# Performance work log

Measured on AMD Instinct MI355X. Metric: run time of the kernel, lower is better.

The kernel has to match this reference:

```python
import jax, jax.numpy as jnp
import numpy as np

N_CONST = 188
P = 16
HIDDEN = 128
DE = 5
DO = 6
N_TARGETS = 5
BATCH = 32


def _edge_indices(n):
    # receiver/sender pairs in the same order as itertools.product, skipping diagonal
    r, s = np.meshgrid(np.arange(n), np.arange(n), indexing='ij')
    mask = r != s
    return jnp.asarray(r[mask]), jnp.asarray(s[mask])  # each [n*(n-1)]


def _linear_params(key, fan_in, fan_out):
    kw, kb = jax.random.split(key)
    w = jax.random.normal(kw, (fan_in, fan_out), jnp.float32) / np.sqrt(fan_in)
    b = jax.random.normal(kb, (fan_out,), jnp.float32) * 0.01
    return w, b


def setup_inputs() -> dict:
    key = jax.random.key(0)
    ks = jax.random.split(key, 10)
    inp = {"x": jax.random.normal(ks[0], (BATCH, N_CONST, P), jnp.float32)}
    h2 = HIDDEN // 2
    dims = [
        ("fr1", 2 * P, HIDDEN), ("fr2", HIDDEN, h2), ("fr3", h2, DE),
        ("fo1", P + DE, HIDDEN), ("fo2", HIDDEN, h2), ("fo3", h2, DO),
        ("fc1", DO * N_CONST, HIDDEN), ("fc2", HIDDEN, h2), ("fc3", h2, N_TARGETS),
    ]
    for i, (name, fi, fo) in enumerate(dims):
        w, b = _linear_params(ks[i + 1], fi, fo)
        inp[name + "_w"] = w
        inp[name + "_b"] = b
    return inp


def reference(x, fr1_w, fr1_b, fr2_w, fr2_b, fr3_w, fr3_b,
              fo1_w, fo1_b, fo2_w, fo2_b, fo3_w, fo3_b,
              fc1_w, fc1_b, fc2_w, fc2_b, fc3_w, fc3_b):
    B, n, p = x.shape
    recv, send = _edge_indices(n)  # [Nr]
    # gather receiver/sender node features (replaces one-hot matmuls with Rr, Rs)
    e_in = jnp.concatenate([x[:, recv], x[:, send]], axis=-1)  # [B, Nr, 2P]
    h = jax.nn.relu(e_in @ fr1_w + fr1_b)
    h = jax.nn.relu(h @ fr2_w + fr2_b)
    E = jax.nn.relu(h @ fr3_w + fr3_b)  # [B, Nr, De]
    # scatter-add edge effects back to receiver nodes (replaces E @ Rr^T)
    Ebar = jnp.zeros((B, n, E.shape[-1]), x.dtype).at[:, recv].add(E)  # [B, N, De]
    c = jnp.concatenate([x, Ebar], axis=-1)  # [B, N, P+De]
    h = jax.nn.relu(c @ fo1_w + fo1_b)
    h = jax.nn.relu(h @ fo2_w + fo2_b)
    O = jax.nn.relu(h @ fo3_w + fo3_b)  # [B, N, Do]
    h = jax.nn.relu(O.reshape(B, -1) @ fc1_w + fc1_b)
    h = jax.nn.relu(h @ fc2_w + fc2_b)
    return h @ fc3_w + fc3_b  # [B, n_targets]
```

## Files before the change

kernel.cpp:

```cpp
#include <hip/hip_runtime.h>

#define BB   32
#define NN   188
#define PP   16
#define HID  128
#define HH2  64
#define DE   5
#define DO   6
#define NT   5
#define ROWS_O (BB*NN)
#define RT   32
#define KO   (PP+DE)

typedef __attribute__((ext_vector_type(8))) short short8;
typedef __attribute__((ext_vector_type(4))) float float4_;
typedef __attribute__((ext_vector_type(4))) unsigned uint4_;

__device__ __forceinline__ short f2bf(float v) {
    union { float f; unsigned u; } a; a.f = v;
    unsigned r = a.u + 0x7fff + ((a.u >> 16) & 1);
    return (short)(r >> 16);
}
__device__ __forceinline__ unsigned relu_pk(float lo, float hi) {
    float l = lo > 0.f ? lo : 0.f;
    float h = hi > 0.f ? hi : 0.f;
    unsigned r;
    asm("v_cvt_pk_bf16_f32 %0, %1, %2" : "=v"(r) : "v"(l), "v"(h));
    return r;
}

#define XB_OFF    0
#define XB_ELTS   (BB*NN*24)
#define W1S_OFF   (XB_OFF + XB_ELTS)
#define W1S_ELTS  (8*64*8)
#define W2S_OFF   (W1S_OFF + W1S_ELTS)
#define W2S_ELTS  (16*64*8)
#define W3S_OFF   (W2S_OFF + W2S_ELTS)
#define W3S_ELTS  (2*64*8)
#define SHORT_TOTAL (W3S_OFF + W3S_ELTS)

__device__ __forceinline__ int kmap(int q, int e) {
    return (e < 4) ? (q*4 + e) : (16 + q*4 + (e - 4));
}

__global__ void prep_kernel(const float* __restrict__ x,
                            const float* __restrict__ w1,
                            const float* __restrict__ w2,
                            const float* __restrict__ w3,
                            short* __restrict__ ws)
{
    const int i = blockIdx.x * blockDim.x + threadIdx.x;
    const int stride = gridDim.x * blockDim.x;
    for (int idx = i; idx < BB*NN*PP; idx += stride) {
        int row = idx >> 4, k = idx & 15;
        ws[XB_OFF + row*24 + k] = f2bf(x[idx]);
    }
    for (int idx = i; idx < W1S_ELTS; idx += stride) {
        int t = idx >> 9;
        int l = (idx >> 3) & 63;
        int e = idx & 7;
        int q = l >> 4, n16 = l & 15;
        ws[W1S_OFF + idx] = f2bf(w1[(q*8 + e)*HID + t*16 + n16]);
    }
    for (int idx = i; idx < W2S_ELTS; idx += stride) {
        int f = idx >> 9;
        int l = (idx >> 3) & 63;
        int e = idx & 7;
        int tt = f >> 2, s = f & 3;
        int q = l >> 4, n16 = l & 15;
        int k = 32*s + kmap(q, e);
        int n = tt*16 + n16;
        ws[W2S_OFF + idx] = f2bf(w2[k*HH2 + n]);
    }
    for (int idx = i; idx < W3S_ELTS; idx += stride) {
        int s2 = idx >> 9;
        int l = (idx >> 3) & 63;
        int e = idx & 7;
        int q = l >> 4, n16 = l & 15;
        int k = 32*s2 + kmap(q, e);
        ws[W3S_OFF + idx] = (n16 < DE) ? f2bf(w3[k*DE + n16]) : (short)0;
    }
}

#define EDGE_TILE(E1C, MASKED, TI)                                              \
    {                                                                           \
        float4_ C2[4];                                                          \
        {    \
            float4_ Ca = __builtin_amdgcn_mfma_f32_16x16x32_bf16(W1f[0], (E1C), cbv[0], 0, 0, 0); \
            float4_ Cb = __builtin_amdgcn_mfma_f32_16x16x32_bf16(W1f[1], (E1C), cbv[1], 0, 0, 0); \
            uint4_ dv = (uint4_){ relu_pk(Ca[0], Ca[1]), relu_pk(Ca[2], Ca[3]),  \
                                  relu_pk(Cb[0], Cb[1]), relu_pk(Cb[2], Cb[3]) };\
            short8 Bf = __builtin_bit_cast(short8, dv);                         \
            C2[0] = __builtin_amdgcn_mfma_f32_16x16x32_bf16(W2f[0],  Bf, bias2v[0], 0, 0, 0); \
            C2[1] = __builtin_amdgcn_mfma_f32_16x16x32_bf16(W2f[4],  Bf, bias2v[1], 0, 0, 0); \
            C2[2] = __builtin_amdgcn_mfma_f32_16x16x32_bf16(W2f[8],  Bf, bias2v[2], 0, 0, 0); \
            C2[3] = __builtin_amdgcn_mfma_f32_16x16x32_bf16(W2f[12], Bf, bias2v[3], 0, 0, 0); \
        }                                                                       \
        _Pragma("unroll")                                                       \
        for (int s = 1; s < 4; ++s) {                                           \
            float4_ Ca = __builtin_amdgcn_mfma_f32_16x16x32_bf16(W1f[2*s],   (E1C), cbv[2*s],   0, 0, 0); \
            float4_ Cb = __builtin_amdgcn_mfma_f32_16x16x32_bf16(W1f[2*s+1], (E1C), cbv[2*s+1], 0, 0, 0); \
            uint4_ dv = (uint4_){ relu_pk(Ca[0], Ca[1]), relu_pk(Ca[2], Ca[3]),  \
                                  relu_pk(Cb[0], Cb[1]), relu_pk(Cb[2], Cb[3]) };\
            short8 Bf = __builtin_bit_cast(short8, dv);                         \
            C2[0] = __builtin_amdgcn_mfma_f32_16x16x32_bf16(W2f[s],    Bf, C2[0], 0, 0, 0); \
            C2[1] = __builtin_amdgcn_mfma_f32_16x16x32_bf16(W2f[4+s],  Bf, C2[1], 0, 0, 0); \
            C2[2] = __builtin_amdgcn_mfma_f32_16x16x32_bf16(W2f[8+s],  Bf, C2[2], 0, 0, 0); \
            C2[3] = __builtin_amdgcn_mfma_f32_16x16x32_bf16(W2f[12+s], Bf, C2[3], 0, 0, 0); \
        }                                                                       \
        float4_ C3;                                                             \
        {               \
            uint4_ dv = (uint4_){ relu_pk(C2[0][0], C2[0][1]), relu_pk(C2[0][2], C2[0][3]), \
                                  relu_pk(C2[1][0], C2[1][1]), relu_pk(C2[1][2], C2[1][3]) }; \
            short8 B3f = __builtin_bit_cast(short8, dv);                        \
            C3 = __builtin_amdgcn_mfma_f32_16x16x32_bf16(W3f[0], B3f, bias3r, 0, 0, 0); \
        }                                                                       \
        {                                                                       \
            uint4_ dv = (uint4_){ relu_pk(C2[2][0], C2[2][1]), relu_pk(C2[2][2], C2[2][3]), \
                                  relu_pk(C2[3][0], C2[3][1]), relu_pk(C2[3][2], C2[3][3]) }; \
            short8 B3f = __builtin_bit_cast(short8, dv);                        \
            C3 = __builtin_amdgcn_mfma_f32_16x16x32_bf16(W3f[1], B3f, C3, 0, 0, 0); \
        }                                                                       \
        if (MASKED) {                       \
            const bool ok = ((TI)*16 + n16 < NN-1);                             \
            _Pragma("unroll")                                                   \
            for (int rg = 0; rg < 4; ++rg) {                                    \
                float v = C3[rg] > 0.f ? C3[rg] : 0.f;                          \
                acc[rg] += ok ? v : 0.f;                                        \
            }                                                                   \
        } else {                                                                \
            _Pragma("unroll")                                                   \
            for (int rg = 0; rg < 4; ++rg)                                      \
                acc[rg] += C3[rg] > 0.f ? C3[rg] : 0.f;                         \
        }                                                                       \
    }

__global__ __launch_bounds__(256) __attribute__((amdgpu_waves_per_eu(2, 2)))
void edge_mfma_kernel(const short* __restrict__ ws_s,
                      const float* __restrict__ b1,
                      const float* __restrict__ b2,
                      const float* __restrict__ b3,
                      float* __restrict__ ebar)
{
    const short* xb  = ws_s + XB_OFF;
    const short* w1g = ws_s + W1S_OFF;
    const short* w2g = ws_s + W2S_OFF;
    const short* w3g = ws_s + W3S_OFF;

    const int tid  = threadIdx.x;
    const int wave = tid >> 6;
    const int lane = tid & 63;
    const int n16  = lane & 15;
    const int q    = lane >> 4;
    const int bi   = blockIdx.x * 4 + wave;
    const int b    = bi / NN;
    const int recv = bi - b*NN;

    short8 W1f[8];
    #pragma unroll
    for (int t = 0; t < 8; ++t)
        W1f[t] = *(const short8*)(w1g + t*512 + lane*8);
    short8 W2f[16];
    #pragma unroll
    for (int f = 0; f < 16; ++f)
        W2f[f] = *(const short8*)(w2g + f*512 + lane*8);
    short8 W3f[2];
    #pragma unroll
    for (int s = 0; s < 2; ++s)
        W3f[s] = *(const short8*)(w3g + s*512 + lane*8);
    float4_ cbv[8];
    #pragma unroll
    for (int t = 0; t < 8; ++t)
        cbv[t] = *(const float4_*)(b1 + t*16 + q*4);
    float4_ bias2v[4];
    #pragma unroll
    for (int tt = 0; tt < 4; ++tt)
        bias2v[tt] = *(const float4_*)(b2 + tt*16 + q*4);
    float4_ bias3r;
    #pragma unroll
    for (int rg = 0; rg < 4; ++rg) {
        int o = q*4 + rg;
        bias3r[rg] = (o < DE) ? b3[o] : 0.f;
    }

    const short* xrow = xb + b*(NN*24);
    const bool rside = (q < 2);

    float acc[4] = {0.f, 0.f, 0.f, 0.f};

    short8 E1;
    {
        int send0 = n16 + (n16 >= recv ? 1 : 0);
        const int node = rside ? recv : send0;
        E1 = *(const short8*)(xrow + node*24 + (q & 1)*8);
    }

    #pragma unroll 1
    for (int ti = 0; ti < 11; ++ti) {
        short8 E1c = E1;
        {
            int en = (ti+1)*16 + n16;
            int send = en + (en >= recv ? 1 : 0);
            if (send > NN-1) send = NN-1;
            const int node = rside ? recv : send;
            E1 = *(const short8*)(xrow + node*24 + (q & 1)*8);
        }
        EDGE_TILE(E1c, false, ti)
    }
    EDGE_TILE(E1, true, 11)

    #pragma unroll
    for (int rg = 0; rg < 4; ++rg) {
        acc[rg] += __shfl_xor(acc[rg], 1);
        acc[rg] += __shfl_xor(acc[rg], 2);
        acc[rg] += __shfl_xor(acc[rg], 4);
        acc[rg] += __shfl_xor(acc[rg], 8);
    }
    if (n16 == 0) {
        #pragma unroll
        for (int rg = 0; rg < 4; ++rg) {
            int o = q*4 + rg;
            if (o < DE) ebar[bi*DE + o] = acc[rg];
        }
    }
}

__global__ __launch_bounds__(512)
void obj_mlp_kernel(const float* __restrict__ x, const float* __restrict__ ebar,
                    const float* __restrict__ w1, const float* __restrict__ b1,
                    const float* __restrict__ w2, const float* __restrict__ b2,
                    const float* __restrict__ w3, const float* __restrict__ b3,
                    float* __restrict__ o_out)
{
    __shared__ float sW[HID*HH2];
    __shared__ float sB1[HID];
    __shared__ float sB2[HH2];
    __shared__ float sCin[RT*KO];
    __shared__ float sH1[RT*HID];
    __shared__ float sH2t[HH2*(RT+1)];
    const int tid = threadIdx.x;
    const int rbase = blockIdx.x * RT;

    for (int i = tid; i < KO*HID; i += 512) sW[i] = w1[i];
    if (tid < HID) sB1[tid] = b1[tid];
    else if (tid < HID+HH2) sB2[tid-HID] = b2[tid-HID];
    for (int i = tid; i < RT*KO; i += 512) {
        int r = i / KO, k = i - r*KO;
        int gr = rbase + r;
        int b = gr / NN;
        int node = gr - b*NN;
        sCin[i] = (k < PP) ? x[(b*NN+node)*PP + k]
                           : ebar[(b*NN+node)*DE + (k-PP)];
    }
    __syncthreads();

    {
        const int j = tid & (HID-1);
        const int g = tid >> 7;
        float w[KO];
        #pragma unroll
        for (int k = 0; k < KO; ++k) w[k] = sW[k*HID + j];
        const float bj = sB1[j];
        #pragma unroll
        for (int rr = 0; rr < 8; ++rr) {
            const int r = g*8 + rr;
            const float* e = &sCin[r*KO];
            float a0=0.f,a1=0.f,a2=0.f;
            #pragma unroll
            for (int k = 0; k < KO; k += 3) {
                a0 += w[k+0]*e[k+0];
                a1 += w[k+1]*e[k+1];
                a2 += w[k+2]*e[k+2];
            }
            float v = a0+a1+a2+bj;
            sH1[r*HID + j] = v > 0.f ? v : 0.f;
        }
    }
    __syncthreads();
    for (int i = tid; i < HID*HH2; i += 512) sW[i] = w2[i];
    __syncthreads();

    {
        const int j = tid & (HH2-1);
        const int g = tid >> 6;
        float acc[4];
        #pragma unroll
        for (int rr = 0; rr < 4; ++rr) acc[rr] = sB2[j];
        #pragma unroll
        for (int kc = 0; kc < HID; kc += 32) {
            float w[32];
            #pragma unroll
            for (int kk = 0; kk < 32; ++kk) w[kk] = sW[(kc+kk)*HH2 + j];
            #pragma unroll
            for (int rr = 0; rr < 4; ++rr) {
                const float* h = &sH1[(g*4+rr)*HID + kc];
                float a0=0.f,a1=0.f,a2=0.f,a3=0.f;
                #pragma unroll
                for (int kk = 0; kk < 32; kk += 4) {
                    a0 += w[kk+0]*h[kk+0];
                    a1 += w[kk+1]*h[kk+1];
                    a2 += w[kk+2]*h[kk+2];
                    a3 += w[kk+3]*h[kk+3];
                }
                acc[rr] += (a0+a1)+(a2+a3);
            }
        }
        #pragma unroll
        for (int rr = 0; rr < 4; ++rr) {
            float v = acc[rr];
            sH2t[j*(RT+1) + (g*4+rr)] = v > 0.f ? v : 0.f;
        }
    }
    __syncthreads();

    if (tid < RT*DO) {
        const int r = tid & (RT-1);
        const int c = tid >> 5;
        float a0=0.f,a1=0.f,a2=0.f,a3=0.f;
        #pragma unroll
        for (int k = 0; k < HH2; k += 4) {
            a0 += sH2t[(k+0)*(RT+1)+r]*w3[(k+0)*DO+c];
            a1 += sH2t[(k+1)*(RT+1)+r]*w3[(k+1)*DO+c];
            a2 += sH2t[(k+2)*(RT+1)+r]*w3[(k+2)*DO+c];
            a3 += sH2t[(k+3)*(RT+1)+r]*w3[(k+3)*DO+c];
        }
        float v = (a0+a1)+(a2+a3) + b3[c];
        v = v > 0.f ? v : 0.f;
        int gr = rbase + r;
        int b = gr / NN;
        int node = gr - b*NN;
        o_out[b*(NN*DO) + node*DO + c] = v;
    }
}

__global__ __launch_bounds__(256)
void fc_kernel(const float* __restrict__ o_in,
               const float* __restrict__ w1, const float* __restrict__ b1,
               const float* __restrict__ w2, const float* __restrict__ b2,
               const float* __restrict__ w3, const float* __restrict__ b3,
               float* __restrict__ out)
{
    __shared__ __align__(16) float s_in[NN*DO];
    __shared__ float s_p[256];
    __shared__ float s_h1[HID];
    __shared__ float s_h2[HH2];
    const int b = blockIdx.x, tid = threadIdx.x;

    for (int i = tid; i < NN*DO; i += 256) s_in[i] = o_in[b*(NN*DO) + i];
    __syncthreads();

    {
        const int j = tid & (HID-1);
        const int h = tid >> 7;
        const float4* s4 = (const float4*)&s_in[h*564];
        const float* wbase = w1 + (size_t)(h*564)*HID + j;
        float a0=0.f,a1=0.f,a2=0.f,a3=0.f;
        #pragma unroll 4
        for (int i = 0; i < 141; ++i) {
            float4 v = s4[i];
            const float* wp = wbase + (size_t)i*4*HID;
            a0 += v.x * wp[0];
            a1 += v.y * wp[HID];
            a2 += v.z * wp[2*HID];
            a3 += v.w * wp[3*HID];
        }
        s_p[tid] = (a0+a1)+(a2+a3);
    }
    __syncthreads();
    if (tid < HID) {
        float v = s_p[tid] + s_p[tid+HID] + b1[tid];
        s_h1[tid] = v > 0.f ? v : 0.f;
    }
    __syncthreads();

    {
        const int j = tid & (HH2-1);
        const int q = tid >> 6;
        float acc = 0.f;
        #pragma unroll
        for (int kk = 0; kk < 32; ++kk) {
            int k = q*32 + kk;
            acc += s_h1[k] * w2[k*HH2 + j];
        }
        s_p[tid] = acc;
    }
    __syncthreads();
    if (tid < HH2) {
        float v = s_p[tid] + s_p[tid+64] + s_p[tid+128] + s_p[tid+192] + b2[tid];
        s_h2[tid] = v > 0.f ? v : 0.f;
    }
    __syncthreads();

    if (tid < NT) {
        float acc = b3[tid];
        #pragma unroll
        for (int k = 0; k < HH2; ++k)
            acc += s_h2[k] * w3[k*NT + tid];
        out[b*NT + tid] = acc;
    }
}

extern "C" void kernel_launch(void* const* d_in, const int* in_sizes, int n_in,
                              void* d_out, int out_size, void* d_ws, size_t ws_size,
                              hipStream_t stream) {
    (void)in_sizes; (void)n_in; (void)out_size; (void)ws_size;
    const float* x     = (const float*)d_in[0];
    const float* fr1_w = (const float*)d_in[1];
    const float* fr1_b = (const float*)d_in[2];
    const float* fr2_w = (const float*)d_in[3];
    const float* fr2_b = (const float*)d_in[4];
    const float* fr3_w = (const float*)d_in[5];
    const float* fr3_b = (const float*)d_in[6];
    const float* fo1_w = (const float*)d_in[7];
    const float* fo1_b = (const float*)d_in[8];
    const float* fo2_w = (const float*)d_in[9];
    const float* fo2_b = (const float*)d_in[10];
    const float* fo3_w = (const float*)d_in[11];
    const float* fo3_b = (const float*)d_in[12];
    const float* fc1_w = (const float*)d_in[13];
    const float* fc1_b = (const float*)d_in[14];
    const float* fc2_w = (const float*)d_in[15];
    const float* fc2_b = (const float*)d_in[16];
    const float* fc3_w = (const float*)d_in[17];
    const float* fc3_b = (const float*)d_in[18];

    short* ws_s = (short*)d_ws;
    size_t fbase = ((size_t)SHORT_TOTAL*2 + 15) & ~(size_t)15;
    float* ebar = (float*)((char*)d_ws + fbase);
    float* o_ws = ebar + BB*NN*DE;

    prep_kernel<<<128, 256, 0, stream>>>(x, fr1_w, fr2_w, fr3_w, ws_s);
    edge_mfma_kernel<<<(BB*NN)/4, 256, 0, stream>>>(ws_s, fr1_b, fr2_b, fr3_b, ebar);
    obj_mlp_kernel<<<ROWS_O/RT, 512, 0, stream>>>(
        x, ebar, fo1_w, fo1_b, fo2_w, fo2_b, fo3_w, fo3_b, o_ws);
    fc_kernel<<<BB, 256, 0, stream>>>(
        o_ws, fc1_w, fc1_b, fc2_w, fc2_b, fc3_w, fc3_b, (float*)d_out);
}
```

Before: 161.2 us.

## Fuse edge, object and fc stages into one persistent kernel with grid barriers

Merges the edge MLP, object MLP and final fc kernels into one persistent kernel of 256 blocks that loops over work and uses software grid-wide barriers built on atomics between stages. The goal is to remove two kernel launches and the gaps between them. In exchange, the edge stage has fewer waves in flight, since each wave now handles up to 6 receivers and the waves_per_eu hint is dropped. The object-MLP stage also shrinks from 32-row tiles on 512 threads to 16-row tiles on 256 threads and reloads its weights into shared memory for every chunk. The grid barrier assumes all 256 blocks are co-resident, which could deadlock if occupancy is insufficient.

Result: slower. 296.8 us (+84.2%).

```diff
diff --git a/kernel.cpp b/kernel.cpp
--- a/kernel.cpp
+++ b/kernel.cpp
@@ -9,8 +9,9 @@
 #define DO   6
 #define NT   5
 #define ROWS_O (BB*NN)
-#define RT   32
+#define RTO  16
 #define KO   (PP+DE)
+#define NBLK 256
 
 typedef __attribute__((ext_vector_type(8))) short short8;
 typedef __attribute__((ext_vector_type(4))) float float4_;
@@ -27,6 +28,9 @@
     unsigned r;
     asm("v_cvt_pk_bf16_f32 %0, %1, %2" : "=v"(r) : "v"(l), "v"(h));
     return r;
+}
+__device__ __forceinline__ float4_ mfma16(short8 a, short8 b, float4_ c) {
+    return __builtin_amdgcn_mfma_f32_16x16x32_bf16(a, b, c, 0, 0, 0);
 }
 
 #define XB_OFF    0
@@ -43,14 +47,34 @@
     return (e < 4) ? (q*4 + e) : (16 + q*4 + (e - 4));
 }
 
+__device__ __forceinline__ void grid_sync(int* bar) {
+    __threadfence();
+    __syncthreads();
+    if (threadIdx.x == 0) {
+        int gen = __hip_atomic_load(bar + 1, __ATOMIC_RELAXED, __HIP_MEMORY_SCOPE_AGENT);
+        int prev = __hip_atomic_fetch_add(bar, 1, __ATOMIC_ACQ_REL, __HIP_MEMORY_SCOPE_AGENT);
+        if (prev == (int)gridDim.x - 1) {
+            __hip_atomic_store(bar, 0, __ATOMIC_RELAXED, __HIP_MEMORY_SCOPE_AGENT);
+            __hip_atomic_fetch_add(bar + 1, 1, __ATOMIC_RELEASE, __HIP_MEMORY_SCOPE_AGENT);
+        } else {
+            while (__hip_atomic_load(bar + 1, __ATOMIC_ACQUIRE, __HIP_MEMORY_SCOPE_AGENT) == gen)
+                __builtin_amdgcn_s_sleep(2);
+        }
+    }
+    __syncthreads();
+    __threadfence();
+}
+
 __global__ void prep_kernel(const float* __restrict__ x,
                             const float* __restrict__ w1,
                             const float* __restrict__ w2,
                             const float* __restrict__ w3,
-                            short* __restrict__ ws)
+                            short* __restrict__ ws,
+                            int* __restrict__ bar)
 {
     const int i = blockIdx.x * blockDim.x + threadIdx.x;
     const int stride = gridDim.x * blockDim.x;
+    if (i == 0) { bar[0] = 0; bar[1] = 0; }
     for (int idx = i; idx < BB*NN*PP; idx += stride) {
         int row = idx >> 4, k = idx & 15;
         ws[XB_OFF + row*24 + k] = f2bf(x[idx]);
@@ -85,43 +109,41 @@
 #define EDGE_TILE(E1C, MASKED, TI)                                              \
     {                                                                           \
         float4_ C2[4];                                                          \
-        {    \
-            float4_ Ca = __builtin_amdgcn_mfma_f32_16x16x32_bf16(W1f[0], (E1C), cbv[0], 0, 0, 0); \
-            float4_ Cb = __builtin_amdgcn_mfma_f32_16x16x32_bf16(W1f[1], (E1C), cbv[1], 0, 0, 0); \
+        {                                                                       \
+            float4_ Ca = mfma16(W1f[0], (E1C), cbv[0]);                         \
+            float4_ Cb = mfma16(W1f[1], (E1C), cbv[1]);                         \
             uint4_ dv = (uint4_){ relu_pk(Ca[0], Ca[1]), relu_pk(Ca[2], Ca[3]),  \
                                   relu_pk(Cb[0], Cb[1]), relu_pk(Cb[2], Cb[3]) };\
             short8 Bf = __builtin_bit_cast(short8, dv);                         \
-            C2[0] = __builtin_amdgcn_mfma_f32_16x16x32_bf16(W2f[0],  Bf, bias2v[0], 0, 0, 0); \
-            C2[1] = __builtin_amdgcn_mfma_f32_16x16x32_bf16(W2f[4],  Bf, bias2v[1], 0, 0, 0); \
-            C2[2] = __builtin_amdgcn_mfma_f32_16x16x32_bf16(W2f[8],  Bf, bias2v[2], 0, 0, 0); \
-            C2[3] = __builtin_amdgcn_mfma_f32_16x16x32_bf16(W2f[12], Bf, bias2v[3], 0, 0, 0); \
+            C2[0] = mfma16(W2f[0],  Bf, bias2v[0]);                             \
+            C2[1] = mfma16(W2f[4],  Bf, bias2v[1]);                             \
+            C2[2] = mfma16(W2f[8],  Bf, bias2v[2]);                             \
+            C2[3] = mfma16(W2f[12], Bf, bias2v[3]);                             \
         }                                                                       \
         _Pragma("unroll")                                                       \
         for (int s = 1; s < 4; ++s) {                                           \
-            float4_ Ca = __builtin_amdgcn_mfma_f32_16x16x32_bf16(W1f[2*s],   (E1C), cbv[2*s],   0, 0, 0); \
-            float4_ Cb = __builtin_amdgcn_mfma_f32_16x16x32_bf16(W1f[2*s+1], (E1C), cbv[2*s+1], 0, 0, 0); \
+            float4_ Ca = mfma16(W1f[2*s],   (E1C), cbv[2*s]);                   \
+            float4_ Cb = mfma16(W1f[2*s+1], (E1C), cbv[2*s+1]);                 \
             uint4_ dv = (uint4_){ relu_pk(Ca[0], Ca[1]), relu_pk(Ca[2], Ca[3]),  \
                                   relu_pk(Cb[0], Cb[1]), relu_pk(Cb[2], Cb[3]) };\
             short8 Bf = __builtin_bit_cast(short8, dv);                         \
-            C2[0] = __builtin_amdgcn_mfma_f32_16x16x32_bf16(W2f[s],    Bf, C2[0], 0, 0, 0); \
-            C2[1] = __builtin_amdgcn_mfma_f32_16x16x32_bf16(W2f[4+s],  Bf, C2[1], 0, 0, 0); \
-            C2[2] = __builtin_amdgcn_mfma_f32_16x16x32_bf16(W2f[8+s],  Bf, C2[2], 0, 0, 0); \
-            C2[3] = __builtin_amdgcn_mfma_f32_16x16x32_bf16(W2f[12+s], Bf, C2[3], 0, 0, 0); \
+            C2[0] = mfma16(W2f[s],    Bf, C2[0]);                               \
+            C2[1] = mfma16(W2f[4+s],  Bf, C2[1]);                               \
+            C2[2] = mfma16(W2f[8+s],  Bf, C2[2]);                               \
+            C2[3] = mfma16(W2f[12+s], Bf, C2[3]);                               \
         }                                                                       \
         float4_ C3;                                                             \
-        {               \
+        {                                                                       \
             uint4_ dv = (uint4_){ relu_pk(C2[0][0], C2[0][1]), relu_pk(C2[0][2], C2[0][3]), \
                                   relu_pk(C2[1][0], C2[1][1]), relu_pk(C2[1][2], C2[1][3]) }; \
-            short8 B3f = __builtin_bit_cast(short8, dv);                        \
-            C3 = __builtin_amdgcn_mfma_f32_16x16x32_bf16(W3f[0], B3f, bias3r, 0, 0, 0); \
+            C3 = mfma16(W3f[0], __builtin_bit_cast(short8, dv), bias3r);        \
         }                                                                       \
         {                                                                       \
             uint4_ dv = (uint4_){ relu_pk(C2[2][0], C2[2][1]), relu_pk(C2[2][2], C2[2][3]), \
                                   relu_pk(C2[3][0], C2[3][1]), relu_pk(C2[3][2], C2[3][3]) }; \
-            short8 B3f = __builtin_bit_cast(short8, dv);                        \
-            C3 = __builtin_amdgcn_mfma_f32_16x16x32_bf16(W3f[1], B3f, C3, 0, 0, 0); \
+            C3 = mfma16(W3f[1], __builtin_bit_cast(short8, dv), C3);            \
         }                                                                       \
-        if (MASKED) {                       \
+        if (MASKED) {                                                           \
             const bool ok = ((TI)*16 + n16 < NN-1);                             \
             _Pragma("unroll")                                                   \
             for (int rg = 0; rg < 4; ++rg) {                                    \
@@ -135,268 +157,279 @@
         }                                                                       \
     }
 
-__global__ __launch_bounds__(256) __attribute__((amdgpu_waves_per_eu(2, 2)))
-void edge_mfma_kernel(const short* __restrict__ ws_s,
-                      const float* __restrict__ b1,
-                      const float* __restrict__ b2,
-                      const float* __restrict__ b3,
-                      float* __restrict__ ebar)
+__global__ __launch_bounds__(256)
+void fused_kernel(const short* __restrict__ ws_s,
+                  const float* __restrict__ fr1_b,
+                  const float* __restrict__ fr2_b,
+                  const float* __restrict__ fr3_b,
+                  float* __restrict__ ebar,
+                  const float* __restrict__ x,
+                  const float* __restrict__ fo1_w, const float* __restrict__ fo1_b,
+                  const float* __restrict__ fo2_w, const float* __restrict__ fo2_b,
+                  const float* __restrict__ fo3_w, const float* __restrict__ fo3_b,
+                  float* __restrict__ o_ws,
+                  const float* __restrict__ fc1_w, const float* __restrict__ fc1_b,
+                  const float* __restrict__ fc2_w, const float* __restrict__ fc2_b,
+                  const float* __restrict__ fc3_w, const float* __restrict__ fc3_b,
+                  float* __restrict__ out,
+                  int* __restrict__ bar)
 {
-    const short* xb  = ws_s + XB_OFF;
-    const short* w1g = ws_s + W1S_OFF;
-    const short* w2g = ws_s + W2S_OFF;
-    const short* w3g = ws_s + W3S_OFF;
+    __shared__ float sW[HID*HH2];
+    __shared__ float sB1[HID];
+    __shared__ float sB2[HH2];
+    __shared__ float sCin[RTO*KO];
+    __shared__ float sH1[RTO*HID];
+    __shared__ float sH2t[HH2*(RTO+1)];
+    __shared__ __align__(16) float s_in[NN*DO];
+    __shared__ float s_p[256];
+    __shared__ float s_h1[HID];
+    __shared__ float s_h2[HH2];
 
     const int tid  = threadIdx.x;
     const int wave = tid >> 6;
     const int lane = tid & 63;
     const int n16  = lane & 15;
     const int q    = lane >> 4;
-    const int bi   = blockIdx.x * 4 + wave;
-    const int b    = bi / NN;
-    const int recv = bi - b*NN;
-
-    short8 W1f[8];
-    #pragma unroll
-    for (int t = 0; t < 8; ++t)
-        W1f[t] = *(const short8*)(w1g + t*512 + lane*8);
-    short8 W2f[16];
-    #pragma unroll
-    for (int f = 0; f < 16; ++f)
-        W2f[f] = *(const short8*)(w2g + f*512 + lane*8);
-    short8 W3f[2];
-    #pragma unroll
-    for (int s = 0; s < 2; ++s)
-        W3f[s] = *(const short8*)(w3g + s*512 + lane*8);
-    float4_ cbv[8];
-    #pragma unroll
-    for (int t = 0; t < 8; ++t)
-        cbv[t] = *(const float4_*)(b1 + t*16 + q*4);
-    float4_ bias2v[4];
-    #pragma unroll
-    for (int tt = 0; tt < 4; ++tt)
-        bias2v[tt] = *(const float4_*)(b2 + tt*16 + q*4);
-    float4_ bias3r;
-    #pragma unroll
-    for (int rg = 0; rg < 4; ++rg) {
-        int o = q*4 + rg;
-        bias3r[rg] = (o < DE) ? b3[o] : 0.f;
-    }
-
-    const short* xrow = xb + b*(NN*24);
-    const bool rside = (q < 2);
-
-    float acc[4] = {0.f, 0.f, 0.f, 0.f};
-
-    short8 E1;
+
     {
-        int send0 = n16 + (n16 >= recv ? 1 : 0);
-        const int node = rside ? recv : send0;
-        E1 = *(const short8*)(xrow + node*24 + (q & 1)*8);
-    }
-
-    #pragma unroll 1
-    for (int ti = 0; ti < 11; ++ti) {
-        short8 E1c = E1;
-        {
-            int en = (ti+1)*16 + n16;
-            int send = en + (en >= recv ? 1 : 0);
-            if (send > NN-1) send = NN-1;
-            const int node = rside ? recv : send;
-            E1 = *(const short8*)(xrow + node*24 + (q & 1)*8);
-        }
-        EDGE_TILE(E1c, false, ti)
-    }
-    EDGE_TILE(E1, true, 11)
-
-    #pragma unroll
-    for (int rg = 0; rg < 4; ++rg) {
-        acc[rg] += __shfl_xor(acc[rg], 1);
-        acc[rg] += __shfl_xor(acc[rg], 2);
-        acc[rg] += __shfl_xor(acc[rg], 4);
-        acc[rg] += __shfl_xor(acc[rg], 8);
-    }
-    if (n16 == 0) {
+        const short* xb  = ws_s + XB_OFF;
+        const short* w1g = ws_s + W1S_OFF;
+        const short* w2g = ws_s + W2S_OFF;
+        const short* w3g = ws_s + W3S_OFF;
+
+        short8 W1f[8];
+        #pragma unroll
+        for (int t = 0; t < 8; ++t)
+            W1f[t] = *(const short8*)(w1g + t*512 + lane*8);
+        short8 W2f[16];
+        #pragma unroll
+        for (int f = 0; f < 16; ++f)
+            W2f[f] = *(const short8*)(w2g + f*512 + lane*8);
+        short8 W3f[2];
+        #pragma unroll
+        for (int s = 0; s < 2; ++s)
+            W3f[s] = *(const short8*)(w3g + s*512 + lane*8);
+        float4_ cbv[8];
+        #pragma unroll
+        for (int t = 0; t < 8; ++t)
+            cbv[t] = *(const float4_*)(fr1_b + t*16 + q*4);
+        float4_ bias2v[4];
+        #pragma unroll
+        for (int tt = 0; tt < 4; ++tt)
+            bias2v[tt] = *(const float4_*)(fr2_b + tt*16 + q*4);
+        float4_ bias3r;
         #pragma unroll
         for (int rg = 0; rg < 4; ++rg) {
             int o = q*4 + rg;
-            if (o < DE) ebar[bi*DE + o] = acc[rg];
-        }
-    }
-}
-
-__global__ __launch_bounds__(512)
-void obj_mlp_kernel(const float* __restrict__ x, const float* __restrict__ ebar,
-                    const float* __restrict__ w1, const float* __restrict__ b1,
-                    const float* __restrict__ w2, const float* __restrict__ b2,
-                    const float* __restrict__ w3, const float* __restrict__ b3,
-                    float* __restrict__ o_out)
-{
-    __shared__ float sW[HID*HH2];
-    __shared__ float sB1[HID];
-    __shared__ float sB2[HH2];
-    __shared__ float sCin[RT*KO];
-    __shared__ float sH1[RT*HID];
-    __shared__ float sH2t[HH2*(RT+1)];
-    const int tid = threadIdx.x;
-    const int rbase = blockIdx.x * RT;
-
-    for (int i = tid; i < KO*HID; i += 512) sW[i] = w1[i];
-    if (tid < HID) sB1[tid] = b1[tid];
-    else if (tid < HID+HH2) sB2[tid-HID] = b2[tid-HID];
-    for (int i = tid; i < RT*KO; i += 512) {
-        int r = i / KO, k = i - r*KO;
-        int gr = rbase + r;
-        int b = gr / NN;
-        int node = gr - b*NN;
-        sCin[i] = (k < PP) ? x[(b*NN+node)*PP + k]
-                           : ebar[(b*NN+node)*DE + (k-PP)];
-    }
-    __syncthreads();
-
-    {
-        const int j = tid & (HID-1);
-        const int g = tid >> 7;
-        float w[KO];
-        #pragma unroll
-        for (int k = 0; k < KO; ++k) w[k] = sW[k*HID + j];
-        const float bj = sB1[j];
-        #pragma unroll
-        for (int rr = 0; rr < 8; ++rr) {
-            const int r = g*8 + rr;
-            const float* e = &sCin[r*KO];
-            float a0=0.f,a1=0.f,a2=0.f;
-            #pragma unroll
-            for (int k = 0; k < KO; k += 3) {
-                a0 += w[k+0]*e[k+0];
-                a1 += w[k+1]*e[k+1];
-                a2 += w[k+2]*e[k+2];
-            }
-            float v = a0+a1+a2+bj;
-            sH1[r*HID + j] = v > 0.f ? v : 0.f;
-        }
-    }
-    __syncthreads();
-    for (int i = tid; i < HID*HH2; i += 512) sW[i] = w2[i];
-    __syncthreads();
-
-    {
-        const int j = tid & (HH2-1);
-        const int g = tid >> 6;
-        float acc[4];
-        #pragma unroll
-        for (int rr = 0; rr < 4; ++rr) acc[rr] = sB2[j];
-        #pragma unroll
-        for (int kc = 0; kc < HID; kc += 32) {
-            float w[32];
-            #pragma unroll
-            for (int kk = 0; kk < 32; ++kk) w[kk] = sW[(kc+kk)*HH2 + j];
+            bias3r[rg] = (o < DE) ? fr3_b[o] : 0.f;
+        }
+        const bool rside = (q < 2);
+        const int qoff = (q & 1)*8;
+        const int gwave = blockIdx.x*4 + wave;
+
+        #pragma unroll 1
+        for (int j = 0; j < 6; ++j) {
+            const int bi = gwave + j*1024;
+            if (bi < ROWS_O) {
+                const int b    = bi / NN;
+                const int recv = bi - b*NN;
+                const short* xrow = xb + b*(NN*24);
+                float acc[4] = {0.f, 0.f, 0.f, 0.f};
+
+                short8 E1;
+                {
+                    int send0 = n16 + (n16 >= recv ? 1 : 0);
+                    const int node = rside ? recv : send0;
+                    E1 = *(const short8*)(xrow + node*24 + qoff);
+                }
+                #pragma unroll 1
+                for (int ti = 0; ti < 11; ++ti) {
+                    short8 E1c = E1;
+                    {
+                        int en = (ti+1)*16 + n16;
+                        int send = en + (en >= recv ? 1 : 0);
+                        if (send > NN-1) send = NN-1;
+                        const int node = rside ? recv : send;
+                        E1 = *(const short8*)(xrow + node*24 + qoff);
+                    }
+                    EDGE_TILE(E1c, false, ti)
+                }
+                EDGE_TILE(E1, true, 11)
+
+                #pragma unroll
+                for (int rg = 0; rg < 4; ++rg) {
+                    acc[rg] += __shfl_xor(acc[rg], 1);
+                    acc[rg] += __shfl_xor(acc[rg], 2);
+                    acc[rg] += __shfl_xor(acc[rg], 4);
+                    acc[rg] += __shfl_xor(acc[rg], 8);
+                }
+                if (n16 == 0) {
+                    #pragma unroll
+                    for (int rg = 0; rg < 4; ++rg) {
+                        int o = q*4 + rg;
+                        if (o < DE) ebar[bi*DE + o] = acc[rg];
+                    }
+                }
+            }
+        }
+    }
+
+    grid_sync(bar);
+
+    #pragma unroll 1
+    for (int chunk = blockIdx.x; chunk < ROWS_O/RTO; chunk += gridDim.x) {
+        const int rbase = chunk * RTO;
+
+        for (int i = tid; i < KO*HID; i += 256) sW[i] = fo1_w[i];
+        if (tid < HID) sB1[tid] = fo1_b[tid];
+        else if (tid < HID+HH2) sB2[tid-HID] = fo2_b[tid-HID];
+        for (int i = tid; i < RTO*KO; i += 256) {
+            int r = i / KO, k = i - r*KO;
+            int gr = rbase + r;
+            int b = gr / NN;
+            int node = gr - b*NN;
+            sCin[i] = (k < PP) ? x[(b*NN+node)*PP + k]
+                               : ebar[(b*NN+node)*DE + (k-PP)];
+        }
+        __syncthreads();
+
+        {
+            const int j = tid & (HID-1);
+            const int g = tid >> 7;
+            float w[KO];
+            #pragma unroll
+            for (int k = 0; k < KO; ++k) w[k] = sW[k*HID + j];
+            const float bj = sB1[j];
+            #pragma unroll
+            for (int rr = 0; rr < 8; ++rr) {
+                const int r = g*8 + rr;
+                const float* e = &sCin[r*KO];
+                float a0=0.f,a1=0.f,a2=0.f;
+                #pragma unroll
+                for (int k = 0; k < KO; k += 3) {
+                    a0 += w[k+0]*e[k+0];
+                    a1 += w[k+1]*e[k+1];
+                    a2 += w[k+2]*e[k+2];
+                }
+                float v = a0+a1+a2+bj;
+                sH1[r*HID + j] = v > 0.f ? v : 0.f;
+            }
+        }
+        __syncthreads();
+        for (int i = tid; i < HID*HH2; i += 256) sW[i] = fo2_w[i];
+        __syncthreads();
+
+        {
+            const int j = tid & (HH2-1);
+            const int g = tid >> 6;
+            float acc2[4];
+            #pragma unroll
+            for (int rr = 0; rr < 4; ++rr) acc2[rr] = sB2[j];
+            #pragma unroll
+            for (int kc = 0; kc < HID; kc += 32) {
+                float w[32];
+                #pragma unroll
+                for (int kk = 0; kk < 32; ++kk) w[kk] = sW[(kc+kk)*HH2 + j];
+                #pragma unroll
+                for (int rr = 0; rr < 4; ++rr) {
+                    const float* h = &sH1[(g*4+rr)*HID + kc];
+                    float a0=0.f,a1=0.f,a2=0.f,a3=0.f;
+                    #pragma unroll
+                    for (int kk = 0; kk < 32; kk += 4) {
+                        a0 += w[kk+0]*h[kk+0];
+                        a1 += w[kk+1]*h[kk+1];
+                        a2 += w[kk+2]*h[kk+2];
+                        a3 += w[kk+3]*h[kk+3];
+                    }
+                    acc2[rr] += (a0+a1)+(a2+a3);
+                }
+            }
             #pragma unroll
             for (int rr = 0; rr < 4; ++rr) {
-                const float* h = &sH1[(g*4+rr)*HID + kc];
-                float a0=0.f,a1=0.f,a2=0.f,a3=0.f;
-                #pragma unroll
-                for (int kk = 0; kk < 32; kk += 4) {
-                    a0 += w[kk+0]*h[kk+0];
-                    a1 += w[kk+1]*h[kk+1];
-                    a2 += w[kk+2]*h[kk+2];
-                    a3 += w[kk+3]*h[kk+3];
-                }
-                acc[rr] += (a0+a1)+(a2+a3);
-            }
-        }
-        #pragma unroll
-        for (int rr = 0; rr < 4; ++rr) {
-            float v = acc[rr];
-            sH2t[j*(RT+1) + (g*4+rr)] = v > 0.f ? v : 0.f;
-        }
-    }
-    __syncthreads();
-
-    if (tid < RT*DO) {
-        const int r = tid & (RT-1);
-        const int c = tid >> 5;
-        float a0=0.f,a1=0.f,a2=0.f,a3=0.f;
-        #pragma unroll
-        for (int k = 0; k < HH2; k += 4) {
-            a0 += sH2t[(k+0)*(RT+1)+r]*w3[(k+0)*DO+c];
-            a1 += sH2t[(k+1)*(RT+1)+r]*w3[(k+1)*DO+c];
-            a2 += sH2t[(k+2)*(RT+1)+r]*w3[(k+2)*DO+c];
-            a3 += sH2t[(k+3)*(RT+1)+r]*w3[(k+3)*DO+c];
-        }
-        float v = (a0+a1)+(a2+a3) + b3[c];
-        v = v > 0.f ? v : 0.f;
-        int gr = rbase + r;
-        int b = gr / NN;
-        int node = gr - b*NN;
-        o_out[b*(NN*DO) + node*DO + c] = v;
-    }
-}
-
-__global__ __launch_bounds__(256)
-void fc_kernel(const float* __restrict__ o_in,
-               const float* __restrict__ w1, const float* __restrict__ b1,
-               const float* __restrict__ w2, const float* __restrict__ b2,
-               const float* __restrict__ w3, const float* __restrict__ b3,
-               float* __restrict__ out)
-{
-    __shared__ __align__(16) float s_in[NN*DO];
-    __shared__ float s_p[256];
-    __shared__ float s_h1[HID];
-    __shared__ float s_h2[HH2];
-    const int b = blockIdx.x, tid = threadIdx.x;
-
-    for (int i = tid; i < NN*DO; i += 256) s_in[i] = o_in[b*(NN*DO) + i];
-    __syncthreads();
-
-    {
-        const int j = tid & (HID-1);
-        const int h = tid >> 7;
-        const float4* s4 = (const float4*)&s_in[h*564];
-        const float* wbase = w1 + (size_t)(h*564)*HID + j;
-        float a0=0.f,a1=0.f,a2=0.f,a3=0.f;
-        #pragma unroll 4
-        for (int i = 0; i < 141; ++i) {
-            float4 v = s4[i];
-            const float* wp = wbase + (size_t)i*4*HID;
-            a0 += v.x * wp[0];
-            a1 += v.y * wp[HID];
-            a2 += v.z * wp[2*HID];
-            a3 += v.w * wp[3*HID];
-        }
-        s_p[tid] = (a0+a1)+(a2+a3);
-    }
-    __syncthreads();
-    if (tid < HID) {
-        float v = s_p[tid] + s_p[tid+HID] + b1[tid];
-        s_h1[tid] = v > 0.f ? v : 0.f;
-    }
-    __syncthreads();
-
-    {
-        const int j = tid & (HH2-1);
-        const int q = tid >> 6;
-        float acc = 0.f;
-        #pragma unroll
-        for (int kk = 0; kk < 32; ++kk) {
-            int k = q*32 + kk;
-            acc += s_h1[k] * w2[k*HH2 + j];
-        }
-        s_p[tid] = acc;
-    }
-    __syncthreads();
-    if (tid < HH2) {
-        float v = s_p[tid] + s_p[tid+64] + s_p[tid+128] + s_p[tid+192] + b2[tid];
-        s_h2[tid] = v > 0.f ? v : 0.f;
-    }
-    __syncthreads();
-
-    if (tid < NT) {
-        float acc = b3[tid];
-        #pragma unroll
-        for (int k = 0; k < HH2; ++k)
-            acc += s_h2[k] * w3[k*NT + tid];
-        out[b*NT + tid] = acc;
+                float v = acc2[rr];
+                sH2t[j*(RTO+1) + (g*4+rr)] = v > 0.f ? v : 0.f;
+            }
+        }
+        __syncthreads();
+
+        if (tid < RTO*DO) {
+            const int r = tid & (RTO-1);
+            const int c = tid >> 4;
+            float a0=0.f,a1=0.f,a2=0.f,a3=0.f;
+            #pragma unroll
+            for (int k = 0; k < HH2; k += 4) {
+                a0 += sH2t[(k+0)*(RTO+1)+r]*fo3_w[(k+0)*DO+c];
+                a1 += sH2t[(k+1)*(RTO+1)+r]*fo3_w[(k+1)*DO+c];
+                a2 += sH2t[(k+2)*(RTO+1)+r]*fo3_w[(k+2)*DO+c];
+                a3 += sH2t[(k+3)*(RTO+1)+r]*fo3_w[(k+3)*DO+c];
+            }
+            float v = (a0+a1)+(a2+a3) + fo3_b[c];
+            v = v > 0.f ? v : 0.f;
+            int gr = rbase + r;
+            int b = gr / NN;
+            int node = gr - b*NN;
+            o_ws[b*(NN*DO) + node*DO + c] = v;
+        }
+        __syncthreads();
+    }
+
+    grid_sync(bar);
+
+    if (blockIdx.x < BB) {
+        const int b = blockIdx.x;
+
+        for (int i = tid; i < NN*DO; i += 256) s_in[i] = o_ws[b*(NN*DO) + i];
+        __syncthreads();
+
+        {
+            const int j = tid & (HID-1);
+            const int h = tid >> 7;
+            const float4* s4 = (const float4*)&s_in[h*564];
+            const float* wbase = fc1_w + (size_t)(h*564)*HID + j;
+            float a0=0.f,a1=0.f,a2=0.f,a3=0.f;
+            #pragma unroll 4
+            for (int i = 0; i < 141; ++i) {
+                float4 v = s4[i];
+                const float* wp = wbase + (size_t)i*4*HID;
+                a0 += v.x * wp[0];
+                a1 += v.y * wp[HID];
+                a2 += v.z * wp[2*HID];
+                a3 += v.w * wp[3*HID];
+            }
+            s_p[tid] = (a0+a1)+(a2+a3);
+        }
+        __syncthreads();
+        if (tid < HID) {
+            float v = s_p[tid] + s_p[tid+HID] + fc1_b[tid];
+            s_h1[tid] = v > 0.f ? v : 0.f;
+        }
+        __syncthreads();
+
+        {
+            const int j = tid & (HH2-1);
+            const int qq = tid >> 6;
+            float acc3 = 0.f;
+            #pragma unroll
+            for (int kk = 0; kk < 32; ++kk) {
+                int k = qq*32 + kk;
+                acc3 += s_h1[k] * fc2_w[k*HH2 + j];
+            }
+            s_p[tid] = acc3;
+        }
+        __syncthreads();
+        if (tid < HH2) {
+            float v = s_p[tid] + s_p[tid+64] + s_p[tid+128] + s_p[tid+192] + fc2_b[tid];
+            s_h2[tid] = v > 0.f ? v : 0.f;
+        }
+        __syncthreads();
+
+        if (tid < NT) {
+            float acc3 = fc3_b[tid];
+            #pragma unroll
+            for (int k = 0; k < HH2; ++k)
+                acc3 += s_h2[k] * fc3_w[k*NT + tid];
+            out[b*NT + tid] = acc3;
+        }
     }
 }
 
@@ -428,11 +461,11 @@
     size_t fbase = ((size_t)SHORT_TOTAL*2 + 15) & ~(size_t)15;
     float* ebar = (float*)((char*)d_ws + fbase);
     float* o_ws = ebar + BB*NN*DE;
-
-    prep_kernel<<<128, 256, 0, stream>>>(x, fr1_w, fr2_w, fr3_w, ws_s);
-    edge_mfma_kernel<<<(BB*NN)/4, 256, 0, stream>>>(ws_s, fr1_b, fr2_b, fr3_b, ebar);
-    obj_mlp_kernel<<<ROWS_O/RT, 512, 0, stream>>>(
-        x, ebar, fo1_w, fo1_b, fo2_w, fo2_b, fo3_w, fo3_b, o_ws);
-    fc_kernel<<<BB, 256, 0, stream>>>(
-        o_ws, fc1_w, fc1_b, fc2_w, fc2_b, fc3_w, fc3_b, (float*)d_out);
-}
+    int*   bar  = (int*)(o_ws + BB*NN*DO);
+
+    prep_kernel<<<128, 256, 0, stream>>>(x, fr1_w, fr2_w, fr3_w, ws_s, bar);
+    fused_kernel<<<NBLK, 256, 0, stream>>>(
+        ws_s, fr1_b, fr2_b, fr3_b, ebar,
+        x, fo1_w, fo1_b, fo2_w, fo2_b, fo3_w, fo3_b, o_ws,
+        fc1_w, fc1_b, fc2_w, fc2_b, fc3_w, fc3_b, (float*)d_out, bar);
+}
```

## Split fc1 across more blocks and shrink obj MLP row tile

Applied to the files above, without the earlier changes.

The fc layer is split into two kernels: fc1 now runs on 8 column-group blocks per batch element with a K-split reduction in shared memory, writing h1 to workspace, and a separate fc23 kernel finishes the remaining layers. The object MLP now uses 16-row tiles with 256 threads instead of 32 rows with 512 threads, doubling its grid. Both changes aim to fill more CUs, since the old fc kernel used only 32 blocks. The cost is an extra kernel launch, an h1 round trip through global memory, and more redundant weight staging per block in the object MLP. The edge kernel edits are cosmetic.

After: 148.9 us, median of 2. 1.08x faster.

```diff
diff --git a/kernel.cpp b/kernel.cpp
--- a/kernel.cpp
+++ b/kernel.cpp
@@ -9,7 +9,7 @@
 #define DO   6
 #define NT   5
 #define ROWS_O (BB*NN)
-#define RT   32
+#define RTO  16
 #define KO   (PP+DE)
 
 typedef __attribute__((ext_vector_type(8))) short short8;
@@ -27,6 +27,9 @@
     unsigned r;
     asm("v_cvt_pk_bf16_f32 %0, %1, %2" : "=v"(r) : "v"(l), "v"(h));
     return r;
+}
+__device__ __forceinline__ float4_ mfma16(short8 a, short8 b, float4_ c) {
+    return __builtin_amdgcn_mfma_f32_16x16x32_bf16(a, b, c, 0, 0, 0);
 }
 
 #define XB_OFF    0
@@ -85,43 +88,41 @@
 #define EDGE_TILE(E1C, MASKED, TI)                                              \
     {                                                                           \
         float4_ C2[4];                                                          \
-        {    \
-            float4_ Ca = __builtin_amdgcn_mfma_f32_16x16x32_bf16(W1f[0], (E1C), cbv[0], 0, 0, 0); \
-            float4_ Cb = __builtin_amdgcn_mfma_f32_16x16x32_bf16(W1f[1], (E1C), cbv[1], 0, 0, 0); \
+        {                                                                       \
+            float4_ Ca = mfma16(W1f[0], (E1C), cbv[0]);                         \
+            float4_ Cb = mfma16(W1f[1], (E1C), cbv[1]);                         \
             uint4_ dv = (uint4_){ relu_pk(Ca[0], Ca[1]), relu_pk(Ca[2], Ca[3]),  \
                                   relu_pk(Cb[0], Cb[1]), relu_pk(Cb[2], Cb[3]) };\
             short8 Bf = __builtin_bit_cast(short8, dv);                         \
-            C2[0] = __builtin_amdgcn_mfma_f32_16x16x32_bf16(W2f[0],  Bf, bias2v[0], 0, 0, 0); \
-            C2[1] = __builtin_amdgcn_mfma_f32_16x16x32_bf16(W2f[4],  Bf, bias2v[1], 0, 0, 0); \
-            C2[2] = __builtin_amdgcn_mfma_f32_16x16x32_bf16(W2f[8],  Bf, bias2v[2], 0, 0, 0); \
-            C2[3] = __builtin_amdgcn_mfma_f32_16x16x32_bf16(W2f[12], Bf, bias2v[3], 0, 0, 0); \
+            C2[0] = mfma16(W2f[0],  Bf, bias2v[0]);                             \
+            C2[1] = mfma16(W2f[4],  Bf, bias2v[1]);                             \
+            C2[2] = mfma16(W2f[8],  Bf, bias2v[2]);                             \
+            C2[3] = mfma16(W2f[12], Bf, bias2v[3]);                             \
         }                                                                       \
         _Pragma("unroll")                                                       \
         for (int s = 1; s < 4; ++s) {                                           \
-            float4_ Ca = __builtin_amdgcn_mfma_f32_16x16x32_bf16(W1f[2*s],   (E1C), cbv[2*s],   0, 0, 0); \
-            float4_ Cb = __builtin_amdgcn_mfma_f32_16x16x32_bf16(W1f[2*s+1], (E1C), cbv[2*s+1], 0, 0, 0); \
+            float4_ Ca = mfma16(W1f[2*s],   (E1C), cbv[2*s]);                   \
+            float4_ Cb = mfma16(W1f[2*s+1], (E1C), cbv[2*s+1]);                 \
             uint4_ dv = (uint4_){ relu_pk(Ca[0], Ca[1]), relu_pk(Ca[2], Ca[3]),  \
                                   relu_pk(Cb[0], Cb[1]), relu_pk(Cb[2], Cb[3]) };\
             short8 Bf = __builtin_bit_cast(short8, dv);                         \
-            C2[0] = __builtin_amdgcn_mfma_f32_16x16x32_bf16(W2f[s],    Bf, C2[0], 0, 0, 0); \
-            C2[1] = __builtin_amdgcn_mfma_f32_16x16x32_bf16(W2f[4+s],  Bf, C2[1], 0, 0, 0); \
-            C2[2] = __builtin_amdgcn_mfma_f32_16x16x32_bf16(W2f[8+s],  Bf, C2[2], 0, 0, 0); \
-            C2[3] = __builtin_amdgcn_mfma_f32_16x16x32_bf16(W2f[12+s], Bf, C2[3], 0, 0, 0); \
+            C2[0] = mfma16(W2f[s],    Bf, C2[0]);                               \
+            C2[1] = mfma16(W2f[4+s],  Bf, C2[1]);                               \
+            C2[2] = mfma16(W2f[8+s],  Bf, C2[2]);                               \
+            C2[3] = mfma16(W2f[12+s], Bf, C2[3]);                               \
         }                                                                       \
         float4_ C3;                                                             \
-        {               \
+        {                                                                       \
             uint4_ dv = (uint4_){ relu_pk(C2[0][0], C2[0][1]), relu_pk(C2[0][2], C2[0][3]), \
                                   relu_pk(C2[1][0], C2[1][1]), relu_pk(C2[1][2], C2[1][3]) }; \
-            short8 B3f = __builtin_bit_cast(short8, dv);                        \
-            C3 = __builtin_amdgcn_mfma_f32_16x16x32_bf16(W3f[0], B3f, bias3r, 0, 0, 0); \
+            C3 = mfma16(W3f[0], __builtin_bit_cast(short8, dv), bias3r);        \
         }                                                                       \
         {                                                                       \
             uint4_ dv = (uint4_){ relu_pk(C2[2][0], C2[2][1]), relu_pk(C2[2][2], C2[2][3]), \
                                   relu_pk(C2[3][0], C2[3][1]), relu_pk(C2[3][2], C2[3][3]) }; \
-            short8 B3f = __builtin_bit_cast(short8, dv);                        \
-            C3 = __builtin_amdgcn_mfma_f32_16x16x32_bf16(W3f[1], B3f, C3, 0, 0, 0); \
+            C3 = mfma16(W3f[1], __builtin_bit_cast(short8, dv), C3);            \
         }                                                                       \
-        if (MASKED) {                       \
+        if (MASKED) {                                                           \
             const bool ok = ((TI)*16 + n16 < NN-1);                             \
             _Pragma("unroll")                                                   \
             for (int rg = 0; rg < 4; ++rg) {                                    \
@@ -185,6 +186,7 @@
 
     const short* xrow = xb + b*(NN*24);
     const bool rside = (q < 2);
+    const int qoff = (q & 1)*8;
 
     float acc[4] = {0.f, 0.f, 0.f, 0.f};
 
@@ -192,7 +194,7 @@
     {
         int send0 = n16 + (n16 >= recv ? 1 : 0);
         const int node = rside ? recv : send0;
-        E1 = *(const short8*)(xrow + node*24 + (q & 1)*8);
+        E1 = *(const short8*)(xrow + node*24 + qoff);
     }
 
     #pragma unroll 1
@@ -203,7 +205,7 @@
             int send = en + (en >= recv ? 1 : 0);
             if (send > NN-1) send = NN-1;
             const int node = rside ? recv : send;
-            E1 = *(const short8*)(xrow + node*24 + (q & 1)*8);
+            E1 = *(const short8*)(xrow + node*24 + qoff);
         }
         EDGE_TILE(E1c, false, ti)
     }
@@ -225,7 +227,7 @@
     }
 }
 
-__global__ __launch_bounds__(512)
+__global__ __launch_bounds__(256)
 void obj_mlp_kernel(const float* __restrict__ x, const float* __restrict__ ebar,
                     const float* __restrict__ w1, const float* __restrict__ b1,
                     const float* __restrict__ w2, const float* __restrict__ b2,
@@ -235,16 +237,16 @@
     __shared__ float sW[HID*HH2];
     __shared__ float sB1[HID];
     __shared__ float sB2[HH2];
-    __shared__ float sCin[RT*KO];
-    __shared__ float sH1[RT*HID];
-    __shared__ float sH2t[HH2*(RT+1)];
+    __shared__ float sCin[RTO*KO];
+    __shared__ float sH1[RTO*HID];
+    __shared__ float sH2t[HH2*(RTO+1)];
     const int tid = threadIdx.x;
-    const int rbase = blockIdx.x * RT;
-
-    for (int i = tid; i < KO*HID; i += 512) sW[i] = w1[i];
+    const int rbase = blockIdx.x * RTO;
+
+    for (int i = tid; i < KO*HID; i += 256) sW[i] = w1[i];
     if (tid < HID) sB1[tid] = b1[tid];
     else if (tid < HID+HH2) sB2[tid-HID] = b2[tid-HID];
-    for (int i = tid; i < RT*KO; i += 512) {
+    for (int i = tid; i < RTO*KO; i += 256) {
         int r = i / KO, k = i - r*KO;
         int gr = rbase + r;
         int b = gr / NN;
@@ -277,7 +279,7 @@
         }
     }
     __syncthreads();
-    for (int i = tid; i < HID*HH2; i += 512) sW[i] = w2[i];
+    for (int i = tid; i < HID*HH2; i += 256) sW[i] = w2[i];
     __syncthreads();
 
     {
@@ -308,21 +310,21 @@
         #pragma unroll
         for (int rr = 0; rr < 4; ++rr) {
             float v = acc[rr];
-            sH2t[j*(RT+1) + (g*4+rr)] = v > 0.f ? v : 0.f;
-        }
-    }
-    __syncthreads();
-
-    if (tid < RT*DO) {
-        const int r = tid & (RT-1);
-        const int c = tid >> 5;
+            sH2t[j*(RTO+1) + (g*4+rr)] = v > 0.f ? v : 0.f;
+        }
+    }
+    __syncthreads();
+
+    if (tid < RTO*DO) {
+        const int r = tid & (RTO-1);
+        const int c = tid >> 4;
         float a0=0.f,a1=0.f,a2=0.f,a3=0.f;
         #pragma unroll
         for (int k = 0; k < HH2; k += 4) {
-            a0 += sH2t[(k+0)*(RT+1)+r]*w3[(k+0)*DO+c];
-            a1 += sH2t[(k+1)*(RT+1)+r]*w3[(k+1)*DO+c];
-            a2 += sH2t[(k+2)*(RT+1)+r]*w3[(k+2)*DO+c];
-            a3 += sH2t[(k+3)*(RT+1)+r]*w3[(k+3)*DO+c];
+            a0 += sH2t[(k+0)*(RTO+1)+r]*w3[(k+0)*DO+c];
+            a1 += sH2t[(k+1)*(RTO+1)+r]*w3[(k+1)*DO+c];
+            a2 += sH2t[(k+2)*(RTO+1)+r]*w3[(k+2)*DO+c];
+            a3 += sH2t[(k+3)*(RTO+1)+r]*w3[(k+3)*DO+c];
         }
         float v = (a0+a1)+(a2+a3) + b3[c];
         v = v > 0.f ? v : 0.f;
@@ -334,43 +336,59 @@
 }
 
 __global__ __launch_bounds__(256)
-void fc_kernel(const float* __restrict__ o_in,
-               const float* __restrict__ w1, const float* __restrict__ b1,
-               const float* __restrict__ w2, const float* __restrict__ b2,
-               const float* __restrict__ w3, const float* __restrict__ b3,
-               float* __restrict__ out)
+void fc1_kernel(const float* __restrict__ o_in,
+                const float* __restrict__ w1, const float* __restrict__ b1,
+                float* __restrict__ h1_ws)
 {
-    __shared__ __align__(16) float s_in[NN*DO];
+    __shared__ __align__(16) float s_o[NN*DO];
+    __shared__ float s_red[16][17];
+    const int tid = threadIdx.x;
+    const int b   = blockIdx.x >> 3;
+    const int cg  = blockIdx.x & 7;
+
+    for (int i = tid; i < NN*DO; i += 256) s_o[i] = o_in[b*(NN*DO) + i];
+    __syncthreads();
+
+    const int col = tid & 15;
+    const int sl  = tid >> 4;
+    const int jg  = cg*16 + col;
+    const int k0  = sl*71;
+    const int k1  = (k0 + 71 < NN*DO) ? k0 + 71 : NN*DO;
+
+    float a0=0.f, a1=0.f, a2=0.f, a3=0.f;
+    int k = k0;
+    for (; k + 3 < k1; k += 4) {
+        a0 += s_o[k+0] * w1[(size_t)(k+0)*HID + jg];
+        a1 += s_o[k+1] * w1[(size_t)(k+1)*HID + jg];
+        a2 += s_o[k+2] * w1[(size_t)(k+2)*HID + jg];
+        a3 += s_o[k+3] * w1[(size_t)(k+3)*HID + jg];
+    }
+    for (; k < k1; ++k)
+        a0 += s_o[k] * w1[(size_t)k*HID + jg];
+    s_red[col][sl] = (a0+a1)+(a2+a3);
+    __syncthreads();
+
+    if (tid < 16) {
+        float t = 0.f;
+        #pragma unroll
+        for (int s = 0; s < 16; ++s) t += s_red[tid][s];
+        t += b1[cg*16 + tid];
+        h1_ws[b*HID + cg*16 + tid] = t > 0.f ? t : 0.f;
+    }
+}
+
+__global__ __launch_bounds__(256)
+void fc23_kernel(const float* __restrict__ h1_ws,
+                 const float* __restrict__ w2, const float* __restrict__ b2,
+                 const float* __restrict__ w3, const float* __restrict__ b3,
+                 float* __restrict__ out)
+{
+    __shared__ float s_h1[HID];
     __shared__ float s_p[256];
-    __shared__ float s_h1[HID];
     __shared__ float s_h2[HH2];
     const int b = blockIdx.x, tid = threadIdx.x;
 
-    for (int i = tid; i < NN*DO; i += 256) s_in[i] = o_in[b*(NN*DO) + i];
-    __syncthreads();
-
-    {
-        const int j = tid & (HID-1);
-        const int h = tid >> 7;
-        const float4* s4 = (const float4*)&s_in[h*564];
-        const float* wbase = w1 + (size_t)(h*564)*HID + j;
-        float a0=0.f,a1=0.f,a2=0.f,a3=0.f;
-        #pragma unroll 4
-        for (int i = 0; i < 141; ++i) {
-            float4 v = s4[i];
-            const float* wp = wbase + (size_t)i*4*HID;
-            a0 += v.x * wp[0];
-            a1 += v.y * wp[HID];
-            a2 += v.z * wp[2*HID];
-            a3 += v.w * wp[3*HID];
-        }
-        s_p[tid] = (a0+a1)+(a2+a3);
-    }
-    __syncthreads();
-    if (tid < HID) {
-        float v = s_p[tid] + s_p[tid+HID] + b1[tid];
-        s_h1[tid] = v > 0.f ? v : 0.f;
-    }
+    if (tid < HID) s_h1[tid] = h1_ws[b*HID + tid];
     __syncthreads();
 
     {
@@ -426,13 +444,15 @@
 
     short* ws_s = (short*)d_ws;
     size_t fbase = ((size_t)SHORT_TOTAL*2 + 15) & ~(size_t)15;
-    float* ebar = (float*)((char*)d_ws + fbase);
-    float* o_ws = ebar + BB*NN*DE;
+    float* ebar  = (float*)((char*)d_ws + fbase);
+    float* o_ws  = ebar + BB*NN*DE;
+    float* h1_ws = o_ws + BB*NN*DO;
 
     prep_kernel<<<128, 256, 0, stream>>>(x, fr1_w, fr2_w, fr3_w, ws_s);
     edge_mfma_kernel<<<(BB*NN)/4, 256, 0, stream>>>(ws_s, fr1_b, fr2_b, fr3_b, ebar);
-    obj_mlp_kernel<<<ROWS_O/RT, 512, 0, stream>>>(
+    obj_mlp_kernel<<<ROWS_O/RTO, 256, 0, stream>>>(
         x, ebar, fo1_w, fo1_b, fo2_w, fo2_b, fo3_w, fo3_b, o_ws);
-    fc_kernel<<<BB, 256, 0, stream>>>(
-        o_ws, fc1_w, fc1_b, fc2_w, fc2_b, fc3_w, fc3_b, (float*)d_out);
-}
+    fc1_kernel<<<BB*8, 256, 0, stream>>>(o_ws, fc1_w, fc1_b, h1_ws);
+    fc23_kernel<<<BB, 256, 0, stream>>>(
+        h1_ws, fc2_w, fc2_b, fc3_w, fc3_b, (float*)d_out);
+}
```
